# Optimization experiments

Measured on AMD Instinct MI355X. Metric: run time of the kernel, lower is better.

Reference implementation:

```python
import jax, jax.numpy as jnp
import numpy as np

B, N, D = 32, 4096, 256      # batch, num input features, input dim
S, H, M = 11, 256, 512       # num_slots, slot_size, mlp_hidden_size
ITERS = 3
ATTN_EPS = 1e-8
LN_EPS = 1e-5


def layer_norm(x, scale, offset):
    mu = jnp.mean(x, axis=-1, keepdims=True)
    var = jnp.var(x, axis=-1, keepdims=True)
    return (x - mu) * scale * jax.lax.rsqrt(var + LN_EPS) + offset


def gru_unroll(updates, w_i, w_h, b):
    # haiku hk.GRU unrolled over axis 1 (time_major=False), zero initial state.
    # updates: [B, T, H]
    h0 = jnp.zeros((updates.shape[0], H), updates.dtype)
    def step(h, x):
        gx = jnp.matmul(x, w_i)                                    # [B, 3H]
        zr = jax.nn.sigmoid(gx[:, :2 * H] + jnp.matmul(h, w_h[:, :2 * H]) + b[:2 * H])
        z, r = zr[:, :H], zr[:, H:]
        a = jnp.tanh(gx[:, 2 * H:] + jnp.matmul(r * h, w_h[:, 2 * H:]) + b[2 * H:])
        h_new = (1.0 - z) * h + z * a
        return h_new, h_new
    _, outs = jax.lax.scan(step, h0, jnp.swapaxes(updates, 0, 1))
    return jnp.swapaxes(outs, 0, 1)                                # [B, T, H]


def setup_inputs():
    key = jax.random.key(0)
    k = jax.random.split(key, 16)
    def lin(kk, fan_in, fan_out):
        return jax.random.normal(kk, (fan_in, fan_out), jnp.float32) / np.sqrt(fan_in).astype(np.float32)
    return {
        "inputs": jax.random.normal(k[0], (B, N, D), jnp.float32),
        "slot_noise": jax.random.normal(k[1], (B, S, H), jnp.float32),
        "ln_in_scale": jnp.ones((D,), jnp.float32),
        "ln_in_offset": jnp.zeros((D,), jnp.float32),
        "ln_slots_scale": jnp.ones((H,), jnp.float32),
        "ln_slots_offset": jnp.zeros((H,), jnp.float32),
        "ln_mlp_scale": jnp.ones((H,), jnp.float32),
        "ln_mlp_offset": jnp.zeros((H,), jnp.float32),
        "slots_mu": jax.random.normal(k[2], (1, 1, H), jnp.float32) * 0.1,
        "slots_log_sigma": jax.random.normal(k[3], (1, 1, H), jnp.float32) * 0.1 - 1.0,
        "Wq": lin(k[4], H, H),
        "Wk": lin(k[5], D, H),
        "Wv": lin(k[6], D, H),
        "gru_wi": lin(k[7], H, 3 * H),
        "gru_wh": lin(k[8], H, 3 * H),
        "gru_b": jnp.zeros((3 * H,), jnp.float32),
        "mlp_w1": lin(k[9], H, M),
        "mlp_b1": jnp.zeros((M,), jnp.float32),
        "mlp_w2": lin(k[10], M, H),
        "mlp_b2": jnp.zeros((H,), jnp.float32),
    }


def reference(inputs, slot_noise, ln_in_scale, ln_in_offset, ln_slots_scale,
              ln_slots_offset, ln_mlp_scale, ln_mlp_offset, slots_mu,
              slots_log_sigma, Wq, Wk, Wv, gru_wi, gru_wh, gru_b,
              mlp_w1, mlp_b1, mlp_w2, mlp_b2):
    x = layer_norm(inputs, ln_in_scale, ln_in_offset)
    kf = jnp.matmul(x, Wk)                                          # [B, N, H]
    vf = jnp.matmul(x, Wv)                                          # [B, N, H]
    slots = slots_mu + jnp.exp(slots_log_sigma) * slot_noise        # [B, S, H]
    scale = H ** (-0.5)
    for _ in range(ITERS):
        q = jnp.matmul(layer_norm(slots, ln_slots_scale, ln_slots_offset), Wq) * scale
        attn_logits = jnp.einsum('bnh,bsh->bns', kf, q)             # [B, N, S]
        attn = jax.nn.softmax(attn_logits, axis=-1) + ATTN_EPS      # softmax over slots
        attn = attn / jnp.sum(attn, axis=-2, keepdims=True)         # normalize over inputs
        updates = jnp.einsum('bns,bnh->bsh', attn, vf)              # [B, S, H]
        slots = gru_unroll(updates, gru_wi, gru_wh, gru_b)          # GRU over slot axis
        mlp_in = layer_norm(slots, ln_mlp_scale, ln_mlp_offset)
        hid = jax.nn.relu(jnp.matmul(mlp_in, mlp_w1) + mlp_b1)
        slots = slots + jnp.matmul(hid, mlp_w2) + mlp_b2
    return slots
```

## Files before the change

### kernel.cpp

```cpp
#include <hip/hip_runtime.h>

typedef unsigned short u16;
typedef __bf16 bf16x8 __attribute__((ext_vector_type(8)));
typedef float  f32x4  __attribute__((ext_vector_type(4)));
typedef unsigned short u16x8 __attribute__((ext_vector_type(8)));

union U8cast { u16x8 u; bf16x8 b; };

#define NB 32
#define NN 4096
#define ND 256
#define NS 11
#define NH 256
#define NM 512

__device__ __forceinline__ u16 f2bf(float f) {
  unsigned u = __float_as_uint(f);
  u += 0x7FFF + ((u >> 16) & 1);
  return (u16)(u >> 16);
}
__device__ __forceinline__ float bf2f(u16 h) {
  return __uint_as_float(((unsigned)h) << 16);
}

__global__ void k_stats_ln(const float* __restrict__ x, const float* __restrict__ sc,
                           const float* __restrict__ of, u16* __restrict__ xbf) {
  int lane = threadIdx.x & 63;
  int wid  = threadIdx.x >> 6;
  int row  = blockIdx.x * 4 + wid;
  float4 v = *(const float4*)(x + (size_t)row * 256 + lane * 4);
  float s1 = v.x + v.y + v.z + v.w;
  float s2 = v.x*v.x + v.y*v.y + v.z*v.z + v.w*v.w;
#pragma unroll
  for (int off = 32; off; off >>= 1) { s1 += __shfl_xor(s1, off); s2 += __shfl_xor(s2, off); }
  float mu = s1 * (1.f/256.f);
  float rs = rsqrtf(s2 * (1.f/256.f) - mu*mu + 1e-5f);
  float4 s4 = *(const float4*)(sc + lane * 4);
  float4 o4 = *(const float4*)(of + lane * 4);
  ushort4 o;
  o.x = f2bf((v.x - mu) * (rs * s4.x) + o4.x);
  o.y = f2bf((v.y - mu) * (rs * s4.y) + o4.y);
  o.z = f2bf((v.z - mu) * (rs * s4.z) + o4.z);
  o.w = f2bf((v.w - mu) * (rs * s4.w) + o4.w);
  *(ushort4*)(xbf + (size_t)row * 256 + lane * 4) = o;
}

__global__ __launch_bounds__(256)
void k_cvt_w(const float* __restrict__ Wk, u16* __restrict__ wT) {
  __shared__ float Lt[64][65];
  int bx = blockIdx.x;
  int kt = bx & 3, ct = bx >> 2;
  int k0 = kt * 64, c0 = ct * 64;
  int t = threadIdx.x;
  int kr = t >> 2, part = t & 3;
  const float* sp = Wk + (size_t)(k0 + kr) * 256 + c0 + part * 16;
#pragma unroll
  for (int g = 0; g < 4; ++g) {
    float4 v = *(const float4*)(sp + g * 4);
    Lt[kr][part*16 + g*4 + 0] = v.x;
    Lt[kr][part*16 + g*4 + 1] = v.y;
    Lt[kr][part*16 + g*4 + 2] = v.z;
    Lt[kr][part*16 + g*4 + 3] = v.w;
  }
  __syncthreads();
  int cr = t >> 2;
  u16* wp = wT + (size_t)(c0 + cr) * 256 + k0 + part * 16;
#pragma unroll
  for (int g = 0; g < 2; ++g) {
    u16x8 o;
#pragma unroll
    for (int j = 0; j < 8; ++j) o[j] = f2bf(Lt[part*16 + g*8 + j][cr]);
    *(u16x8*)(wp + g * 8) = o;
  }
}

__global__ __launch_bounds__(256)
void k_mk(const float* __restrict__ Wq, const u16* __restrict__ wT,
          u16* __restrict__ Mb) {
  __shared__ float xn[256];
  __shared__ float part[8][256];
  int e = blockIdx.x, t = threadIdx.x;
  xn[t] = Wq[e*256 + t];
  __syncthreads();
  int tc = t & 31, kg = t >> 5;
  float a[8] = {};
#pragma unroll 8
  for (int kk = 0; kk < 32; ++kk) {
    int k = kg*32 + kk;
    float xv = xn[k];
    u16x8 wv = *(const u16x8*)(wT + k*256 + tc*8);
#pragma unroll
    for (int j = 0; j < 8; ++j) a[j] += xv * bf2f(wv[j]);
  }
  *(float4*)&part[kg][tc*8]     = make_float4(a[0], a[1], a[2], a[3]);
  *(float4*)&part[kg][tc*8 + 4] = make_float4(a[4], a[5], a[6], a[7]);
  __syncthreads();
  float s = 0.f;
#pragma unroll
  for (int g = 0; g < 8; ++g) s += part[g][t];
  Mb[e*256 + t] = f2bf(s);
}

__global__ __launch_bounds__(384)
void k_wvi(const float* __restrict__ Wv, const float* __restrict__ wi,
           u16* __restrict__ wvib) {
  __shared__ float xn[256];
  __shared__ float part[4][768];
  int d = blockIdx.x, t = threadIdx.x;
  if (t < 256) xn[t] = Wv[d*256 + t];
  __syncthreads();
  int tc = t % 96, kg = t / 96;
  float a[8] = {};
#pragma unroll 4
  for (int kk = 0; kk < 64; ++kk) {
    int k = kg*64 + kk;
    float xv = xn[k];
    float4 w0 = *(const float4*)(wi + (size_t)k*768 + tc*8);
    float4 w1 = *(const float4*)(wi + (size_t)k*768 + tc*8 + 4);
    a[0] += xv * w0.x; a[1] += xv * w0.y; a[2] += xv * w0.z; a[3] += xv * w0.w;
    a[4] += xv * w1.x; a[5] += xv * w1.y; a[6] += xv * w1.z; a[7] += xv * w1.w;
  }
  *(float4*)&part[kg][tc*8]     = make_float4(a[0], a[1], a[2], a[3]);
  *(float4*)&part[kg][tc*8 + 4] = make_float4(a[4], a[5], a[6], a[7]);
  __syncthreads();
#pragma unroll
  for (int c = t; c < 768; c += 384) {
    float s = part[0][c] + part[1][c] + part[2][c] + part[3][c];
    wvib[d*768 + c] = f2bf(s);
  }
}

__global__ void k_cvt_all(const float* __restrict__ wh, const float* __restrict__ w1,
                          const float* __restrict__ w2,
                          const float* __restrict__ noise, const float* __restrict__ smu,
                          const float* __restrict__ sls,
                          u16* __restrict__ whb, u16* __restrict__ w1b,
                          u16* __restrict__ w2b, float* __restrict__ slots) {
  int idx = blockIdx.x * 256 + threadIdx.x;
  if      (idx < 196608) whb[idx]          = f2bf(wh[idx]);
  else if (idx < 327680) w1b[idx - 196608] = f2bf(w1[idx - 196608]);
  else if (idx < 458752) w2b[idx - 327680] = f2bf(w2[idx - 327680]);
  else {
    int i = idx - 458752;
    int c = i & 255;
    slots[i] = smu[c] + expf(sls[c]) * noise[i];
  }
}

__global__ __launch_bounds__(256)
void k_q_ln(const float* __restrict__ slots, const float* __restrict__ sc,
            const float* __restrict__ of, const u16* __restrict__ Mb,
            float* __restrict__ qk2, float* __restrict__ updates,
            float* __restrict__ colsum) {
  __shared__ float xn[256];
  __shared__ float red[8];
  __shared__ float part[8][256];
  int row = blockIdx.x, t = threadIdx.x;
  float v = slots[row*256 + t];
  float s1 = v, s2 = v*v;
#pragma unroll
  for (int off = 32; off; off >>= 1) { s1 += __shfl_xor(s1, off); s2 += __shfl_xor(s2, off); }
  int w = t >> 6;
  if ((t & 63) == 0) { red[w*2] = s1; red[w*2+1] = s2; }
  __syncthreads();
  float a1 = red[0] + red[2] + red[4] + red[6];
  float a2 = red[1] + red[3] + red[5] + red[7];
  float mu = a1 * (1.f/256.f);
  float rs = rsqrtf(a2 * (1.f/256.f) - mu*mu + 1e-5f);
  xn[t] = (v - mu) * rs * sc[t] + of[t];
  updates[row*256 + t] = 0.f;
  if (t == 0) colsum[(row/11)*16 + (row%11)] = 0.f;
  __syncthreads();
  int tc = t & 31, kg = t >> 5;
  float a[8] = {};
#pragma unroll 8
  for (int kk = 0; kk < 32; ++kk) {
    int k = kg*32 + kk;
    float xv = xn[k];
    u16x8 wv = *(const u16x8*)(Mb + k*256 + tc*8);
#pragma unroll
    for (int j = 0; j < 8; ++j) a[j] += xv * bf2f(wv[j]);
  }
  *(float4*)&part[kg][tc*8]     = make_float4(a[0], a[1], a[2], a[3]);
  *(float4*)&part[kg][tc*8 + 4] = make_float4(a[4], a[5], a[6], a[7]);
  __syncthreads();
  float s = 0.f;
#pragma unroll
  for (int g = 0; g < 8; ++g) s += part[g][t];
  qk2[row*256 + t] = s * 0.0625f;
}

__global__ __launch_bounds__(256)
void k_attn_up(const u16* __restrict__ xbf, const float* __restrict__ qg,
               float* __restrict__ updates, float* __restrict__ colsum) {
  __shared__ __align__(16) u16 kfL[64][264];
  __shared__ __align__(16) u16 vfL[64][256];
  __shared__ __align__(16) u16 qTL[16][264];
  __shared__ __align__(16) u16 PTL[16][72];
  __shared__ float Lg[64][17];
  int t = threadIdx.x;
  int b = blockIdx.y;
  int nb0 = blockIdx.x * 256;
  int lane = t & 63, w = t >> 6;
  int fr = lane & 15, kq = lane >> 4;

#pragma unroll
  for (int i = t; i < 512; i += 256) {
    int s = i >> 5, k0 = (i & 31) * 8;
    u16x8 o;
    if (s < 11) {
      const float* qp = qg + (size_t)b*2816 + s*256 + k0;
#pragma unroll
      for (int j = 0; j < 8; ++j) o[j] = f2bf(qp[j]);
    } else {
#pragma unroll
      for (int j = 0; j < 8; ++j) o[j] = 0;
    }
    *(u16x8*)&qTL[s][k0] = o;
  }
  for (int i = t; i < 16*72; i += 256) ((u16*)PTL)[i] = 0;

  f32x4 accU[4] = {};
  float csA[11];
#pragma unroll
  for (int s = 0; s < 11; ++s) csA[s] = 0.f;

  for (int c = 0; c < 4; ++c) {
    int n0 = nb0 + c*64;
    __syncthreads();
    {
      int hc = (t & 31) * 8;
#pragma unroll
      for (int nr = 0; nr < 8; ++nr) {
        int n = nr*8 + (t >> 5);
        size_t base = ((size_t)b*4096 + n0 + n) * 256;
        u16x8 kvk = *(const u16x8*)(xbf + base + hc);
        *(u16x8*)&kfL[n][hc] = kvk;
        *(u16x8*)&vfL[n][hc ^ (((n >> 3) & 3) * 16)] = kvk;
      }
    }
    __syncthreads();
    {
      f32x4 aL = {};
#pragma unroll
      for (int kc = 0; kc < 256; kc += 32) {
        bf16x8 af = *(const bf16x8*)&kfL[w*16 + fr][kc + kq*8];
        bf16x8 bq = *(const bf16x8*)&qTL[fr][kc + kq*8];
        aL = __builtin_amdgcn_mfma_f32_16x16x32_bf16(af, bq, aL, 0, 0, 0);
      }
#pragma unroll
      for (int r = 0; r < 4; ++r)
        Lg[w*16 + kq*4 + r][fr] = aL[r];
    }
    __syncthreads();
    if (t < 64) {
      float p[11];
#pragma unroll
      for (int s = 0; s < 11; ++s) p[s] = Lg[t][s];
      float m = p[0];
#pragma unroll
      for (int s = 1; s < 11; ++s) m = fmaxf(m, p[s]);
      float Z = 0.f;
#pragma unroll
      for (int s = 0; s < 11; ++s) { p[s] = __expf(p[s] - m); Z += p[s]; }
      float iz = 1.f / Z;
#pragma unroll
      for (int s = 0; s < 11; ++s) {
        u16 pb = f2bf(p[s]*iz + 1e-8f);
        csA[s] += bf2f(pb);
        PTL[s][t] = pb;
      }
    }
    __syncthreads();
#pragma unroll
    for (int ht = 0; ht < 4; ++ht) {
      int h = w*64 + ht*16 + fr;
#pragma unroll
      for (int kc = 0; kc < 64; kc += 32) {
        bf16x8 aP = *(const bf16x8*)&PTL[fr][kc + kq*8];
        U8cast bv;
#pragma unroll
        for (int j = 0; j < 8; ++j) {
          int k = kc + kq*8 + j;
          bv.u[j] = vfL[k][h ^ (((k >> 3) & 3) * 16)];
        }
        accU[ht] = __builtin_amdgcn_mfma_f32_16x16x32_bf16(aP, bv.b, accU[ht], 0, 0, 0);
      }
    }
  }
#pragma unroll
  for (int ht = 0; ht < 4; ++ht) {
    int h = w*64 + ht*16 + fr;
#pragma unroll
    for (int r = 0; r < 4; ++r) {
      int s = kq*4 + r;
      if (s < 11)
        atomicAdd(&updates[((size_t)b*11 + s)*256 + h], accU[ht][r]);
    }
  }
  if (t < 64) {
#pragma unroll
    for (int s = 0; s < 11; ++s) {
#pragma unroll
      for (int off = 32; off; off >>= 1) csA[s] += __shfl_xor(csA[s], off);
    }
    if (lane == 0) {
#pragma unroll
      for (int s = 0; s < 11; ++s) atomicAdd(&colsum[b*16 + s], csA[s]);
    }
  }
}

__global__ __launch_bounds__(384)
void k_gx(const float* __restrict__ updates, const float* __restrict__ colsum,
          const u16* __restrict__ wvib, float* __restrict__ gx) {
  __shared__ float xn[256];
  __shared__ float part[4][768];
  int row = blockIdx.x, t = threadIdx.x;
  if (t < 256) {
    float inv = 1.f / colsum[(row/11)*16 + (row%11)];
    xn[t] = updates[row*256 + t] * inv;
  }
  __syncthreads();
  int tc = t % 96, kg = t / 96;
  float a[8] = {};
#pragma unroll 4
  for (int kk = 0; kk < 64; ++kk) {
    int k = kg*64 + kk;
    float xv = xn[k];
    u16x8 wv = *(const u16x8*)(wvib + k*768 + tc*8);
#pragma unroll
    for (int j = 0; j < 8; ++j) a[j] += xv * bf2f(wv[j]);
  }
  *(float4*)&part[kg][tc*8]     = make_float4(a[0], a[1], a[2], a[3]);
  *(float4*)&part[kg][tc*8 + 4] = make_float4(a[4], a[5], a[6], a[7]);
  __syncthreads();
#pragma unroll
  for (int c = t; c < 768; c += 384) {
    float s = part[0][c] + part[1][c] + part[2][c] + part[3][c];
    gx[row*768 + c] = s;
  }
}

__global__ __launch_bounds__(512)
void k_gru(const float* __restrict__ gx, const u16* __restrict__ whb,
           const float* __restrict__ gb, float* __restrict__ slots) {
  __shared__ float h[256], rh[256], zv[256];
  __shared__ float part[4096];
  int b = blockIdx.x, t = threadIdx.x;
  if (t < 256) h[t] = 0.f;
  __syncthreads();
  for (int step = 0; step < 11; ++step) {
    int row = b*11 + step;
    {
      int tc = t & 63, kg = t >> 6;
      float a[8] = {};
#pragma unroll 8
      for (int kk = 0; kk < 32; ++kk) {
        int k = kg*32 + kk;
        float xv = h[k];
        u16x8 wv = *(const u16x8*)(whb + k*768 + tc*8);
#pragma unroll
        for (int j = 0; j < 8; ++j) a[j] += xv * bf2f(wv[j]);
      }
      *(float4*)&part[kg*512 + tc*8]     = make_float4(a[0], a[1], a[2], a[3]);
      *(float4*)&part[kg*512 + tc*8 + 4] = make_float4(a[4], a[5], a[6], a[7]);
    }
    __syncthreads();
    {
      int c = t;
      float s = gx[row*768 + c] + gb[c];
#pragma unroll
      for (int g = 0; g < 8; ++g) s += part[g*512 + c];
      float sg = 1.f / (1.f + __expf(-s));
      if (c < 256) zv[c] = sg;
      else         rh[c - 256] = sg * h[c - 256];
    }
    __syncthreads();
    {
      int tc = t & 31, kg = t >> 5;
      float a[8] = {};
#pragma unroll 8
      for (int kk = 0; kk < 16; ++kk) {
        int k = kg*16 + kk;
        float xv = rh[k];
        u16x8 wv = *(const u16x8*)(whb + k*768 + 512 + tc*8);
#pragma unroll
        for (int j = 0; j < 8; ++j) a[j] += xv * bf2f(wv[j]);
      }
      *(float4*)&part[kg*256 + tc*8]     = make_float4(a[0], a[1], a[2], a[3]);
      *(float4*)&part[kg*256 + tc*8 + 4] = make_float4(a[4], a[5], a[6], a[7]);
    }
    __syncthreads();
    if (t < 256) {
      int c = t;
      float s = gx[row*768 + 512 + c] + gb[512 + c];
#pragma unroll
      for (int g = 0; g < 16; ++g) s += part[g*256 + c];
      float av = tanhf(s);
      float hn = (1.f - zv[c])*h[c] + zv[c]*av;
      h[c] = hn;
      slots[row*256 + c] = hn;
    }
    __syncthreads();
  }
}

__global__ __launch_bounds__(256)
void k_mlp(float* __restrict__ slots, const float* __restrict__ sc,
           const float* __restrict__ of, const u16* __restrict__ w1b,
           const float* __restrict__ b1, const u16* __restrict__ w2b,
           const float* __restrict__ b2, float* __restrict__ out2) {
  __shared__ float xn[256];
  __shared__ float hid[512];
  __shared__ float red[8];
  __shared__ float part[2048];
  int row = blockIdx.x, t = threadIdx.x;
  float v = slots[row*256 + t];
  float s1 = v, s2 = v*v;
#pragma unroll
  for (int off = 32; off; off >>= 1) { s1 += __shfl_xor(s1, off); s2 += __shfl_xor(s2, off); }
  int w = t >> 6;
  if ((t & 63) == 0) { red[w*2] = s1; red[w*2+1] = s2; }
  __syncthreads();
  float a1s = red[0] + red[2] + red[4] + red[6];
  float a2s = red[1] + red[3] + red[5] + red[7];
  float mu = a1s * (1.f/256.f);
  float rs = rsqrtf(a2s * (1.f/256.f) - mu*mu + 1e-5f);
  xn[t] = (v - mu) * rs * sc[t] + of[t];
  __syncthreads();
  {
    int tc = t & 63, kg = t >> 6;
    float a[8] = {};
#pragma unroll 4
    for (int kk = 0; kk < 64; ++kk) {
      int k = kg*64 + kk;
      float xv = xn[k];
      u16x8 wv = *(const u16x8*)(w1b + k*512 + tc*8);
#pragma unroll
      for (int j = 0; j < 8; ++j) a[j] += xv * bf2f(wv[j]);
    }
    *(float4*)&part[kg*512 + tc*8]     = make_float4(a[0], a[1], a[2], a[3]);
    *(float4*)&part[kg*512 + tc*8 + 4] = make_float4(a[4], a[5], a[6], a[7]);
  }
  __syncthreads();
#pragma unroll
  for (int c = t; c < 512; c += 256) {
    float s = b1[c];
#pragma unroll
    for (int g = 0; g < 4; ++g) s += part[g*512 + c];
    hid[c] = fmaxf(s, 0.f);
  }
  __syncthreads();
  {
    int tc = t & 31, kg = t >> 5;
    float a[8] = {};
#pragma unroll 4
    for (int kk = 0; kk < 64; ++kk) {
      int k = kg*64 + kk;
      float xv = hid[k];
      u16x8 wv = *(const u16x8*)(w2b + k*256 + tc*8);
#pragma unroll
      for (int j = 0; j < 8; ++j) a[j] += xv * bf2f(wv[j]);
    }
    *(float4*)&part[kg*256 + tc*8]     = make_float4(a[0], a[1], a[2], a[3]);
    *(float4*)&part[kg*256 + tc*8 + 4] = make_float4(a[4], a[5], a[6], a[7]);
  }
  __syncthreads();
  {
    float s = v + b2[t];
#pragma unroll
    for (int g = 0; g < 8; ++g) s += part[g*256 + t];
    slots[row*256 + t] = s;
    if (out2) out2[row*256 + t] = s;
  }
}

extern "C" void kernel_launch(void* const* d_in, const int* in_sizes, int n_in,
                              void* d_out, int out_size, void* d_ws, size_t ws_size,
                              hipStream_t stream) {
  (void)in_sizes; (void)n_in; (void)out_size; (void)ws_size;
  const float* inputs = (const float*)d_in[0];
  const float* noise  = (const float*)d_in[1];
  const float* lnin_s = (const float*)d_in[2];
  const float* lnin_o = (const float*)d_in[3];
  const float* lnsl_s = (const float*)d_in[4];
  const float* lnsl_o = (const float*)d_in[5];
  const float* lnml_s = (const float*)d_in[6];
  const float* lnml_o = (const float*)d_in[7];
  const float* smu    = (const float*)d_in[8];
  const float* sls    = (const float*)d_in[9];
  const float* Wq     = (const float*)d_in[10];
  const float* Wk     = (const float*)d_in[11];
  const float* Wv     = (const float*)d_in[12];
  const float* gwi    = (const float*)d_in[13];
  const float* gwh    = (const float*)d_in[14];
  const float* gb     = (const float*)d_in[15];
  const float* w1     = (const float*)d_in[16];
  const float* b1     = (const float*)d_in[17];
  const float* w2     = (const float*)d_in[18];
  const float* b2     = (const float*)d_in[19];

  char* ws = (char*)d_ws;
  u16*    wT      = (u16*)(ws + 134217728);
  float*  slots   = (float*)(ws + 139984896);
  float*  updates = (float*)(ws + 140345344);
  float*  gx      = (float*)(ws + 140705792);
  float*  qk2     = (float*)(ws + 140705792);
  float*  colsum  = (float*)(ws + 141787136);
  u16*    Mb      = (u16*)(ws + 141789184);
  u16*    wvib    = (u16*)(ws + 141920256);
  u16*    whb     = (u16*)(ws + 142313472);
  u16*    w1b     = (u16*)(ws + 142706688);
  u16*    w2b     = (u16*)(ws + 142968832);
  u16*    xbf     = (u16*)(ws + 143230976);

  k_stats_ln <<<32768, 256, 0, stream>>>(inputs, lnin_s, lnin_o, xbf);
  k_cvt_w    <<<16,    256, 0, stream>>>(Wk, wT);
  k_mk       <<<256,   256, 0, stream>>>(Wq, wT, Mb);
  k_wvi      <<<256,   384, 0, stream>>>(Wv, gwi, wvib);
  k_cvt_all  <<<2144,  256, 0, stream>>>(gwh, w1, w2, noise, smu, sls,
                                         whb, w1b, w2b, slots);

  for (int it = 0; it < 3; ++it) {
    k_q_ln    <<<352, 256, 0, stream>>>(slots, lnsl_s, lnsl_o, Mb, qk2, updates, colsum);
    k_attn_up <<<dim3(16, 32), 256, 0, stream>>>(xbf, qk2, updates, colsum);
    k_gx      <<<352, 384, 0, stream>>>(updates, colsum, wvib, gx);
    k_gru     <<<32,  512, 0, stream>>>(gx, whb, gb, slots);
    k_mlp     <<<352, 256, 0, stream>>>(slots, lnml_s, lnml_o, w1b, b1, w2b, b2,
                                        (it == 2) ? (float*)d_out : nullptr);
  }
}
```

Before: 548.4 us.

## Fuse gx, GRU, MLP and next-iteration query into one per-batch kernel

```diff
diff --git a/kernel.cpp b/kernel.cpp
--- a/kernel.cpp
+++ b/kernel.cpp
@@ -193,7 +193,6 @@
 __global__ __launch_bounds__(256)
 void k_attn_up(const u16* __restrict__ xbf, const float* __restrict__ qg,
                float* __restrict__ updates, float* __restrict__ colsum) {
-  __shared__ __align__(16) u16 kfL[64][264];
   __shared__ __align__(16) u16 vfL[64][256];
   __shared__ __align__(16) u16 qTL[16][264];
   __shared__ __align__(16) u16 PTL[16][72];
@@ -225,26 +224,30 @@
 #pragma unroll
   for (int s = 0; s < 11; ++s) csA[s] = 0.f;
 
+  int j32  = t & 31;
+  int nsub = t >> 5;
+  int js   = (j32 ^ nsub) * 8;
+  int hc   = j32 * 8;
+
   for (int c = 0; c < 4; ++c) {
     int n0 = nb0 + c*64;
     __syncthreads();
     {
-      int hc = (t & 31) * 8;
 #pragma unroll
       for (int nr = 0; nr < 8; ++nr) {
-        int n = nr*8 + (t >> 5);
+        int n = nr*8 + nsub;
         size_t base = ((size_t)b*4096 + n0 + n) * 256;
         u16x8 kvk = *(const u16x8*)(xbf + base + hc);
-        *(u16x8*)&kfL[n][hc] = kvk;
-        *(u16x8*)&vfL[n][hc ^ (((n >> 3) & 3) * 16)] = kvk;
+        *(u16x8*)&vfL[n][js] = kvk;
       }
     }
     __syncthreads();
     {
       f32x4 aL = {};
+      int n = w*16 + fr;
 #pragma unroll
       for (int kc = 0; kc < 256; kc += 32) {
-        bf16x8 af = *(const bf16x8*)&kfL[w*16 + fr][kc + kq*8];
+        bf16x8 af = *(const bf16x8*)&vfL[n][((kc/8 + kq) ^ (fr & 7)) * 8];
         bf16x8 bq = *(const bf16x8*)&qTL[fr][kc + kq*8];
         aL = __builtin_amdgcn_mfma_f32_16x16x32_bf16(af, bq, aL, 0, 0, 0);
       }
@@ -275,6 +278,7 @@
 #pragma unroll
     for (int ht = 0; ht < 4; ++ht) {
       int h = w*64 + ht*16 + fr;
+      int h3 = h >> 3, h7 = h & 7;
 #pragma unroll
       for (int kc = 0; kc < 64; kc += 32) {
         bf16x8 aP = *(const bf16x8*)&PTL[fr][kc + kq*8];
@@ -282,7 +286,7 @@
 #pragma unroll
         for (int j = 0; j < 8; ++j) {
           int k = kc + kq*8 + j;
-          bv.u[j] = vfL[k][h ^ (((k >> 3) & 3) * 16)];
+          bv.u[j] = vfL[k][((h3 ^ j) << 3) | h7];
         }
         accU[ht] = __builtin_amdgcn_mfma_f32_16x16x32_bf16(aP, bv.b, accU[ht], 0, 0, 0);
       }
@@ -311,55 +315,64 @@
   }
 }
 
-__global__ __launch_bounds__(384)
-void k_gx(const float* __restrict__ updates, const float* __restrict__ colsum,
-          const u16* __restrict__ wvib, float* __restrict__ gx) {
-  __shared__ float xn[256];
-  __shared__ float part[4][768];
-  int row = blockIdx.x, t = threadIdx.x;
-  if (t < 256) {
-    float inv = 1.f / colsum[(row/11)*16 + (row%11)];
-    xn[t] = updates[row*256 + t] * inv;
-  }
-  __syncthreads();
-  int tc = t % 96, kg = t / 96;
-  float a[8] = {};
+__global__ __launch_bounds__(512)
+void k_slot_update(float* __restrict__ updates, float* __restrict__ colsum,
+                   const u16* __restrict__ wvib, const u16* __restrict__ whb,
+                   const float* __restrict__ gb,
+                   const float* __restrict__ mls, const float* __restrict__ mlo,
+                   const u16* __restrict__ w1b, const float* __restrict__ b1,
+                   const u16* __restrict__ w2b, const float* __restrict__ b2,
+                   const float* __restrict__ sls_, const float* __restrict__ slo,
+                   const u16* __restrict__ Mb,
+                   float* __restrict__ qk2, float* __restrict__ out2) {
+  __shared__ float xnAll[11][256];
+  __shared__ float gxL[11][768];
+  __shared__ float part[4096];
+  __shared__ float hsh[256], rhsh[256], zvsh[256];
+  __shared__ float xn2[2][256];
+  __shared__ float hid2[2][512];
+  __shared__ float red2[2][8];
+  __shared__ float invcs[11];
+
+  int b = blockIdx.x, t = threadIdx.x;
+  int row0 = b * 11;
+
+  if (t < 11) invcs[t] = 1.f / colsum[b*16 + t];
+  __syncthreads();
+  if (t < 11) colsum[b*16 + t] = 0.f;
+  for (int i = t; i < 2816; i += 512) {
+    int r = i >> 8, c = i & 255;
+    xnAll[r][c] = updates[(size_t)(row0 + r)*256 + c] * invcs[r];
+    updates[(size_t)(row0 + r)*256 + c] = 0.f;
+  }
+  if (t < 256) hsh[t] = 0.f;
+  __syncthreads();
+
+  for (int g = t; g < 1056; g += 512) {
+    int r = g / 96, c8 = g % 96;
+    const float* xr = xnAll[r];
+    float a[8] = {};
 #pragma unroll 4
-  for (int kk = 0; kk < 64; ++kk) {
-    int k = kg*64 + kk;
-    float xv = xn[k];
-    u16x8 wv = *(const u16x8*)(wvib + k*768 + tc*8);
-#pragma unroll
-    for (int j = 0; j < 8; ++j) a[j] += xv * bf2f(wv[j]);
-  }
-  *(float4*)&part[kg][tc*8]     = make_float4(a[0], a[1], a[2], a[3]);
-  *(float4*)&part[kg][tc*8 + 4] = make_float4(a[4], a[5], a[6], a[7]);
-  __syncthreads();
-#pragma unroll
-  for (int c = t; c < 768; c += 384) {
-    float s = part[0][c] + part[1][c] + part[2][c] + part[3][c];
-    gx[row*768 + c] = s;
-  }
-}
-
-__global__ __launch_bounds__(512)
-void k_gru(const float* __restrict__ gx, const u16* __restrict__ whb,
-           const float* __restrict__ gb, float* __restrict__ slots) {
-  __shared__ float h[256], rh[256], zv[256];
-  __shared__ float part[4096];
-  int b = blockIdx.x, t = threadIdx.x;
-  if (t < 256) h[t] = 0.f;
-  __syncthreads();
+    for (int k = 0; k < 256; ++k) {
+      float xv = xr[k];
+      u16x8 wv = *(const u16x8*)(wvib + (size_t)k*768 + c8*8);
+#pragma unroll
+      for (int j = 0; j < 8; ++j) a[j] += xv * bf2f(wv[j]);
+    }
+#pragma unroll
+    for (int j = 0; j < 8; ++j) gxL[r][c8*8 + j] = a[j];
+  }
+  __syncthreads();
+
   for (int step = 0; step < 11; ++step) {
-    int row = b*11 + step;
     {
       int tc = t & 63, kg = t >> 6;
       float a[8] = {};
 #pragma unroll 8
       for (int kk = 0; kk < 32; ++kk) {
         int k = kg*32 + kk;
-        float xv = h[k];
-        u16x8 wv = *(const u16x8*)(whb + k*768 + tc*8);
+        float xv = hsh[k];
+        u16x8 wv = *(const u16x8*)(whb + (size_t)k*768 + tc*8);
 #pragma unroll
         for (int j = 0; j < 8; ++j) a[j] += xv * bf2f(wv[j]);
       }
@@ -369,12 +382,12 @@
     __syncthreads();
     {
       int c = t;
-      float s = gx[row*768 + c] + gb[c];
+      float s = gxL[step][c] + gb[c];
 #pragma unroll
       for (int g = 0; g < 8; ++g) s += part[g*512 + c];
       float sg = 1.f / (1.f + __expf(-s));
-      if (c < 256) zv[c] = sg;
-      else         rh[c - 256] = sg * h[c - 256];
+      if (c < 256) zvsh[c] = sg;
+      else         rhsh[c - 256] = sg * hsh[c - 256];
     }
     __syncthreads();
     {
@@ -383,8 +396,8 @@
 #pragma unroll 8
       for (int kk = 0; kk < 16; ++kk) {
         int k = kg*16 + kk;
-        float xv = rh[k];
-        u16x8 wv = *(const u16x8*)(whb + k*768 + 512 + tc*8);
+        float xv = rhsh[k];
+        u16x8 wv = *(const u16x8*)(whb + (size_t)k*768 + 512 + tc*8);
 #pragma unroll
         for (int j = 0; j < 8; ++j) a[j] += xv * bf2f(wv[j]);
       }
@@ -394,85 +407,118 @@
     __syncthreads();
     if (t < 256) {
       int c = t;
-      float s = gx[row*768 + 512 + c] + gb[512 + c];
+      float s = gxL[step][512 + c] + gb[512 + c];
 #pragma unroll
       for (int g = 0; g < 16; ++g) s += part[g*256 + c];
       float av = tanhf(s);
-      float hn = (1.f - zv[c])*h[c] + zv[c]*av;
-      h[c] = hn;
-      slots[row*256 + c] = hn;
-    }
-    __syncthreads();
-  }
-}
-
-__global__ __launch_bounds__(256)
-void k_mlp(float* __restrict__ slots, const float* __restrict__ sc,
-           const float* __restrict__ of, const u16* __restrict__ w1b,
-           const float* __restrict__ b1, const u16* __restrict__ w2b,
-           const float* __restrict__ b2, float* __restrict__ out2) {
-  __shared__ float xn[256];
-  __shared__ float hid[512];
-  __shared__ float red[8];
-  __shared__ float part[2048];
-  int row = blockIdx.x, t = threadIdx.x;
-  float v = slots[row*256 + t];
-  float s1 = v, s2 = v*v;
-#pragma unroll
-  for (int off = 32; off; off >>= 1) { s1 += __shfl_xor(s1, off); s2 += __shfl_xor(s2, off); }
-  int w = t >> 6;
-  if ((t & 63) == 0) { red[w*2] = s1; red[w*2+1] = s2; }
-  __syncthreads();
-  float a1s = red[0] + red[2] + red[4] + red[6];
-  float a2s = red[1] + red[3] + red[5] + red[7];
-  float mu = a1s * (1.f/256.f);
-  float rs = rsqrtf(a2s * (1.f/256.f) - mu*mu + 1e-5f);
-  xn[t] = (v - mu) * rs * sc[t] + of[t];
-  __syncthreads();
-  {
-    int tc = t & 63, kg = t >> 6;
-    float a[8] = {};
+      float hn = (1.f - zvsh[c])*hsh[c] + zvsh[c]*av;
+      hsh[c] = hn;
+      xnAll[step][c] = hn;
+    }
+    __syncthreads();
+  }
+
+  int hh = t >> 8;
+  int c  = t & 255;
+  int w4 = (t >> 6) & 3;
+  for (int p = 0; p < 6; ++p) {
+    int r = p*2 + hh;
+    bool valid = (r < 11);
+    float v = valid ? xnAll[r][c] : 0.f;
+    float s1 = v, s2 = v*v;
+#pragma unroll
+    for (int off = 32; off; off >>= 1) { s1 += __shfl_xor(s1, off); s2 += __shfl_xor(s2, off); }
+    if ((t & 63) == 0) { red2[hh][w4*2] = s1; red2[hh][w4*2+1] = s2; }
+    __syncthreads();
+    {
+      float a1 = red2[hh][0] + red2[hh][2] + red2[hh][4] + red2[hh][6];
+      float a2 = red2[hh][1] + red2[hh][3] + red2[hh][5] + red2[hh][7];
+      float mu = a1 * (1.f/256.f);
+      float rs = rsqrtf(a2 * (1.f/256.f) - mu*mu + 1e-5f);
+      xn2[hh][c] = (v - mu) * rs * mls[c] + mlo[c];
+    }
+    __syncthreads();
+    {
+      int tc = c & 63, kg = c >> 6;
+      float a[8] = {};
 #pragma unroll 4
-    for (int kk = 0; kk < 64; ++kk) {
-      int k = kg*64 + kk;
-      float xv = xn[k];
-      u16x8 wv = *(const u16x8*)(w1b + k*512 + tc*8);
-#pragma unroll
-      for (int j = 0; j < 8; ++j) a[j] += xv * bf2f(wv[j]);
-    }
-    *(float4*)&part[kg*512 + tc*8]     = make_float4(a[0], a[1], a[2], a[3]);
-    *(float4*)&part[kg*512 + tc*8 + 4] = make_float4(a[4], a[5], a[6], a[7]);
-  }
-  __syncthreads();
-#pragma unroll
-  for (int c = t; c < 512; c += 256) {
-    float s = b1[c];
-#pragma unroll
-    for (int g = 0; g < 4; ++g) s += part[g*512 + c];
-    hid[c] = fmaxf(s, 0.f);
-  }
-  __syncthreads();
-  {
-    int tc = t & 31, kg = t >> 5;
-    float a[8] = {};
+      for (int kk = 0; kk < 64; ++kk) {
+        int k = kg*64 + kk;
+        float xv = xn2[hh][k];
+        u16x8 wv = *(const u16x8*)(w1b + (size_t)k*512 + tc*8);
+#pragma unroll
+        for (int j = 0; j < 8; ++j) a[j] += xv * bf2f(wv[j]);
+      }
+      *(float4*)&part[hh*2048 + kg*512 + tc*8]     = make_float4(a[0], a[1], a[2], a[3]);
+      *(float4*)&part[hh*2048 + kg*512 + tc*8 + 4] = make_float4(a[4], a[5], a[6], a[7]);
+    }
+    __syncthreads();
+#pragma unroll
+    for (int cc = c; cc < 512; cc += 256) {
+      float s = b1[cc];
+#pragma unroll
+      for (int g = 0; g < 4; ++g) s += part[hh*2048 + g*512 + cc];
+      hid2[hh][cc] = fmaxf(s, 0.f);
+    }
+    __syncthreads();
+    {
+      int tc = c & 31, kg = c >> 5;
+      float a[8] = {};
 #pragma unroll 4
-    for (int kk = 0; kk < 64; ++kk) {
-      int k = kg*64 + kk;
-      float xv = hid[k];
-      u16x8 wv = *(const u16x8*)(w2b + k*256 + tc*8);
-#pragma unroll
-      for (int j = 0; j < 8; ++j) a[j] += xv * bf2f(wv[j]);
-    }
-    *(float4*)&part[kg*256 + tc*8]     = make_float4(a[0], a[1], a[2], a[3]);
-    *(float4*)&part[kg*256 + tc*8 + 4] = make_float4(a[4], a[5], a[6], a[7]);
-  }
-  __syncthreads();
-  {
-    float s = v + b2[t];
-#pragma unroll
-    for (int g = 0; g < 8; ++g) s += part[g*256 + t];
-    slots[row*256 + t] = s;
-    if (out2) out2[row*256 + t] = s;
+      for (int kk = 0; kk < 64; ++kk) {
+        int k = kg*64 + kk;
+        float xv = hid2[hh][k];
+        u16x8 wv = *(const u16x8*)(w2b + (size_t)k*256 + tc*8);
+#pragma unroll
+        for (int j = 0; j < 8; ++j) a[j] += xv * bf2f(wv[j]);
+      }
+      *(float4*)&part[hh*2048 + kg*256 + tc*8]     = make_float4(a[0], a[1], a[2], a[3]);
+      *(float4*)&part[hh*2048 + kg*256 + tc*8 + 4] = make_float4(a[4], a[5], a[6], a[7]);
+    }
+    __syncthreads();
+    float snew;
+    {
+      float s = v + b2[c];
+#pragma unroll
+      for (int g = 0; g < 8; ++g) s += part[hh*2048 + g*256 + c];
+      snew = s;
+      if (valid && out2) out2[(size_t)(row0 + r)*256 + c] = snew;
+    }
+    float q1 = snew, q2 = snew*snew;
+#pragma unroll
+    for (int off = 32; off; off >>= 1) { q1 += __shfl_xor(q1, off); q2 += __shfl_xor(q2, off); }
+    if ((t & 63) == 0) { red2[hh][w4*2] = q1; red2[hh][w4*2+1] = q2; }
+    __syncthreads();
+    {
+      float a1 = red2[hh][0] + red2[hh][2] + red2[hh][4] + red2[hh][6];
+      float a2 = red2[hh][1] + red2[hh][3] + red2[hh][5] + red2[hh][7];
+      float mu = a1 * (1.f/256.f);
+      float rs = rsqrtf(a2 * (1.f/256.f) - mu*mu + 1e-5f);
+      xn2[hh][c] = (snew - mu) * rs * sls_[c] + slo[c];
+    }
+    __syncthreads();
+    {
+      int tc = c & 31, kg = c >> 5;
+      float a[8] = {};
+#pragma unroll 8
+      for (int kk = 0; kk < 32; ++kk) {
+        int k = kg*32 + kk;
+        float xv = xn2[hh][k];
+        u16x8 wv = *(const u16x8*)(Mb + (size_t)k*256 + tc*8);
+#pragma unroll
+        for (int j = 0; j < 8; ++j) a[j] += xv * bf2f(wv[j]);
+      }
+      *(float4*)&part[hh*2048 + kg*256 + tc*8]     = make_float4(a[0], a[1], a[2], a[3]);
+      *(float4*)&part[hh*2048 + kg*256 + tc*8 + 4] = make_float4(a[4], a[5], a[6], a[7]);
+    }
+    __syncthreads();
+    if (valid) {
+      float s = 0.f;
+#pragma unroll
+      for (int g = 0; g < 8; ++g) s += part[hh*2048 + g*256 + c];
+      qk2[(size_t)(row0 + r)*256 + c] = s * 0.0625f;
+    }
+    __syncthreads();
   }
 }
 
@@ -505,7 +551,6 @@
   u16*    wT      = (u16*)(ws + 134217728);
   float*  slots   = (float*)(ws + 139984896);
   float*  updates = (float*)(ws + 140345344);
-  float*  gx      = (float*)(ws + 140705792);
   float*  qk2     = (float*)(ws + 140705792);
   float*  colsum  = (float*)(ws + 141787136);
   u16*    Mb      = (u16*)(ws + 141789184);
@@ -521,13 +566,13 @@
   k_wvi      <<<256,   384, 0, stream>>>(Wv, gwi, wvib);
   k_cvt_all  <<<2144,  256, 0, stream>>>(gwh, w1, w2, noise, smu, sls,
                                          whb, w1b, w2b, slots);
+  k_q_ln     <<<352,   256, 0, stream>>>(slots, lnsl_s, lnsl_o, Mb, qk2, updates, colsum);
 
   for (int it = 0; it < 3; ++it) {
-    k_q_ln    <<<352, 256, 0, stream>>>(slots, lnsl_s, lnsl_o, Mb, qk2, updates, colsum);
-    k_attn_up <<<dim3(16, 32), 256, 0, stream>>>(xbf, qk2, updates, colsum);
-    k_gx      <<<352, 384, 0, stream>>>(updates, colsum, wvib, gx);
-    k_gru     <<<32,  512, 0, stream>>>(gx, whb, gb, slots);
-    k_mlp     <<<352, 256, 0, stream>>>(slots, lnml_s, lnml_o, w1b, b1, w2b, b2,
-                                        (it == 2) ? (float*)d_out : nullptr);
-  }
-}
+    k_attn_up     <<<dim3(16, 32), 256, 0, stream>>>(xbf, qk2, updates, colsum);
+    k_slot_update <<<32, 512, 0, stream>>>(updates, colsum, wvib, whb, gb,
+                                           lnml_s, lnml_o, w1b, b1, w2b, b2,
+                                           lnsl_s, lnsl_o, Mb, qk2,
+                                           (it == 2) ? (float*)d_out : nullptr);
+  }
+}
```

After: 818.4 us. 49.2% more time.
